# Optimization experiments

Hardware: AMD Instinct MI355X
Metric: run time of the kernel (lower is better)

## Reference

```python
import math
import jax, jax.numpy as jnp
import numpy as np

N_MARKS = 64
D_TYPE = 256      # d_type_emb (= d_k since each head module has n_head=1)
D_TIME = 256      # must be even
N_HEAD = 4
N_LAYERS = 3
D_IN = D_TYPE + D_TIME  # input dim to per-layer QKV projections
NEG = -1000000000.0
LN_EPS = 1e-5


def temporal_embedding(time):
    # time: [B,T] -> [B,T,D_TIME]; pe[...,0::2]=sin(t*div), pe[...,1::2]=cos(t*div)
    div_term = jnp.exp(jnp.arange(0, D_TIME, 2, dtype=time.dtype) * (-(math.log(10000.0) / D_TIME)))
    ang = time[..., None] * div_term  # [B,T,D_TIME//2]
    pe = jnp.stack([jnp.sin(ang), jnp.cos(ang)], axis=-1)  # interleave sin/cos
    return pe.reshape(time.shape[0], time.shape[1], D_TIME)


def layer_norm(x, w, b):
    mu = jnp.mean(x, axis=-1, keepdims=True)
    var = jnp.mean(jnp.square(x - mu), axis=-1, keepdims=True)
    return (x - mu) * jax.lax.rsqrt(var + LN_EPS) * w + b


def setup_inputs() -> dict:
    key = jax.random.key(0)
    ks = jax.random.split(key, 12)
    B, T = 4, 1024
    event_seqs = jax.random.uniform(ks[0], (B, T, N_MARKS), dtype=jnp.float32)
    time_seqs = jax.random.uniform(ks[1], (B, T), dtype=jnp.float32)
    non_pad_mask = jnp.ones((B, T, T), dtype=bool)
    s_in = 1.0 / math.sqrt(D_IN)
    s_mk = 1.0 / math.sqrt(N_MARKS)
    Wtype = jax.random.uniform(ks[2], (N_MARKS, D_TYPE), minval=-s_mk, maxval=s_mk)
    btype = jax.random.uniform(ks[3], (D_TYPE,), minval=-s_mk, maxval=s_mk)
    Wq = jax.random.uniform(ks[4], (N_HEAD, N_LAYERS, D_IN, D_TYPE), minval=-s_in, maxval=s_in)
    bq = jax.random.uniform(ks[5], (N_HEAD, N_LAYERS, D_TYPE), minval=-s_in, maxval=s_in)
    Wk = jax.random.uniform(ks[6], (N_HEAD, N_LAYERS, D_IN, D_TYPE), minval=-s_in, maxval=s_in)
    bk = jax.random.uniform(ks[7], (N_HEAD, N_LAYERS, D_TYPE), minval=-s_in, maxval=s_in)
    Wv = jax.random.uniform(ks[8], (N_HEAD, N_LAYERS, D_IN, D_TYPE), minval=-s_in, maxval=s_in)
    bv = jax.random.uniform(ks[9], (N_HEAD, N_LAYERS, D_TYPE), minval=-s_in, maxval=s_in)
    norm_w = jnp.ones((D_TYPE,), dtype=jnp.float32)
    norm_b = jnp.zeros((D_TYPE,), dtype=jnp.float32)
    return {"event_seqs": event_seqs, "time_seqs": time_seqs, "non_pad_mask": non_pad_mask,
            "Wtype": Wtype, "btype": btype, "Wq": Wq, "bq": bq, "Wk": Wk, "bk": bk,
            "Wv": Wv, "bv": bv, "norm_w": norm_w, "norm_b": norm_b}


def reference(event_seqs, time_seqs, non_pad_mask, Wtype, btype, Wq, bq, Wk, bk, Wv, bv, norm_w, norm_b):
    B, T, _ = event_seqs.shape
    # attention mask: True => masked (torch masked_fill(mask > 0, -1e9)); strict+diag upper tri
    tri = jnp.triu(jnp.ones((T, T), dtype=bool))[None]           # [1,T,T]
    attention_mask = tri & non_pad_mask                          # [B,T,T]
    layer_mask = jnp.broadcast_to(~jnp.eye(T, dtype=bool)[None], (B, T, T))
    top = jnp.concatenate([attention_mask, jnp.ones((B, T, T), dtype=bool)], axis=-1)
    bot = jnp.concatenate([attention_mask, layer_mask], axis=-1)
    combined_mask = jnp.concatenate([top, bot], axis=1)          # [B,2T,2T]

    time_emb = temporal_embedding(time_seqs)                     # [B,T,D_TIME]
    type_emb = jnp.tanh(event_seqs @ Wtype + btype)              # [B,T,D_TYPE]
    event_emb = jnp.concatenate([type_emb, time_emb], axis=-1)   # [B,T,D_IN]
    sample_time_emb = time_emb                                   # sample_times=None path
    init_cur = jnp.zeros_like(type_emb)

    scale = 1.0 / math.sqrt(D_TYPE)
    cur_layers = []
    # NOTE: event_emb is sequentially updated across layers AND heads, matching the source.
    for h in range(N_HEAD):
        cur = init_cur
        for l in range(N_LAYERS):
            x = jnp.concatenate([event_emb,
                                 jnp.concatenate([cur, sample_time_emb], axis=-1)], axis=1)  # [B,2T,D_IN]
            q = x @ Wq[h, l] + bq[h, l]
            k = x @ Wk[h, l] + bk[h, l]
            v = x @ Wv[h, l] + bv[h, l]
            scores = jnp.einsum('bqd,bkd->bqk', q, k) * scale    # [B,2T,2T]
            scores = jnp.where(combined_mask, NEG, scores)
            p = jax.nn.softmax(scores, axis=-1)
            out = jnp.einsum('bqk,bkd->bqd', p, v)               # [B,2T,D_TYPE]
            cur = jnp.tanh(out[:, T:, :]) + cur
            event_emb = jnp.concatenate([out[:, :T, :], time_emb], axis=-1)
            cur = layer_norm(cur, norm_w, norm_b)                # use_norm=True
        cur_layers.append(cur)
    return jnp.concatenate(cur_layers, axis=-1)                  # [B,T,D_TYPE*N_HEAD]
```

## Files before the change

kernel.cpp:

```cpp
#include <hip/hip_runtime.h>

typedef __attribute__((ext_vector_type(8))) short short8;
typedef __attribute__((ext_vector_type(4))) float f32x4;
typedef __attribute__((ext_vector_type(4))) unsigned short us4v;
typedef unsigned short ushort_t;
typedef unsigned int uint_t;

#define BB 4
#define T_ 1024
#define T2 2048
#define DD 256
#define DIN 512
#define NMARK 64
#define LNEPS 1e-5f
#define KDIV (-0.035977892078032f)
#define SEGL 8

__device__ __forceinline__ ushort_t f2bf(float f) {
  unsigned int u = __float_as_uint(f);
  unsigned int r = (u + 0x7fffu + ((u >> 16) & 1u)) >> 16;
  return (ushort_t)r;
}
__device__ __forceinline__ uint_t pack2(float a, float b) {
  return (uint_t)f2bf(a) | ((uint_t)f2bf(b) << 16);
}
__device__ __forceinline__ uint_t cvtpk(float lo, float hi) {
  uint_t r;
  asm("v_cvt_pk_bf16_f32 %0, %1, %2" : "=v"(r) : "v"(lo), "v"(hi));
  return r;
}

typedef const __attribute__((address_space(1))) unsigned int* as1cu32;
typedef __attribute__((address_space(3))) unsigned int* as3u32;
__device__ __forceinline__ void async_copy16(const void* g, void* l) {
  __builtin_amdgcn_global_load_lds((as1cu32)g, (as3u32)l, 16, 0, 0);
}

__global__ __launch_bounds__(256) void k_init(const float* __restrict__ ev,
                                              const float* __restrict__ tm,
                                              const float* __restrict__ Wt,
                                              const float* __restrict__ bt,
                                              ushort_t* __restrict__ Xh,
                                              float* __restrict__ Cur) {
  const int btq = blockIdx.x;
  const int b = btq >> 10;
  const int t = btq & 1023;
  const int d = threadIdx.x;
  __shared__ float evs[NMARK];
  if (d < NMARK) evs[d] = ev[(size_t)btq * NMARK + d];
  __syncthreads();
  float s = bt[d];
#pragma unroll
  for (int m = 0; m < NMARK; ++m) s += evs[m] * Wt[m * DD + d];
  const float te_type = tanhf(s);
  const float tv = tm[btq];
  const int i = d >> 1;
  const float dv = expf((float)(2 * i) * KDIV);
  const float ang = tv * dv;
  const float te_time = (d & 1) ? cosf(ang) : sinf(ang);
  ushort_t* Xb = Xh + (size_t)b * T2 * DIN;
  const ushort_t tt = f2bf(te_time);
  Xb[(size_t)t * DIN + d] = f2bf(te_type);
  Xb[(size_t)t * DIN + DD + d] = tt;
  Xb[(size_t)(T_ + t) * DIN + d] = 0;
  Xb[(size_t)(T_ + t) * DIN + DD + d] = tt;
  Cur[((size_t)b * T_ + t) * DD + d] = 0.0f;
}

__global__ __launch_bounds__(256) void k_transW(const float* __restrict__ Wq,
                                                const float* __restrict__ Wk,
                                                const float* __restrict__ Wv,
                                                ushort_t* __restrict__ WT) {
  const int mi = blockIdx.x;
  const int wsel = mi / 12, hl = mi % 12;
  const float* W = ((wsel == 0) ? Wq : (wsel == 1) ? Wk : Wv) + (size_t)hl * DIN * DD;
  const int t = blockIdx.y;
  const int k0 = (t >> 2) * 64, n0 = (t & 3) * 64;
  __shared__ float Ts[64][65];
  const int tid = threadIdx.x;
#pragma unroll
  for (int i = 0; i < 16; ++i) {
    const int idx = tid + i * 256;
    const int r = idx >> 6, c = idx & 63;
    Ts[r][c] = W[(size_t)(k0 + r) * DD + n0 + c];
  }
  __syncthreads();
  ushort_t* D = WT + (size_t)mi * DD * DIN;
#pragma unroll
  for (int i = 0; i < 16; ++i) {
    const int idx = tid + i * 256;
    const int rn = idx >> 6, ck = idx & 63;
    D[(size_t)(n0 + rn) * DIN + k0 + ck] = f2bf(Ts[ck][rn]);
  }
}

__global__ __launch_bounds__(256) void k_qkv(const ushort_t* __restrict__ Xh,
                                             const ushort_t* __restrict__ WT,
                                             const float* __restrict__ bq,
                                             const float* __restrict__ bk,
                                             const float* __restrict__ bv,
                                             ushort_t* __restrict__ Qh,
                                             ushort_t* __restrict__ Kh,
                                             ushort_t* __restrict__ VTt,
                                             int hl) {
  const int m0 = blockIdx.x * 128;
  const int n0 = blockIdx.y * 128;
  const int wsel = blockIdx.z;
  const ushort_t* Bt = WT + ((size_t)(wsel * 12 + hl)) * DD * DIN + (size_t)n0 * DIN;
  const float* bias = (wsel == 0) ? bq : (wsel == 1) ? bk : bv;

  __shared__ ushort_t As[128 * 64];
  __shared__ ushort_t Bs[128 * 64];
  const int tid = threadIdx.x;
  const int w = tid >> 6, lane = tid & 63;
  const int wr = w >> 1, wc = w & 1;
  const int lr = lane & 15, kg = lane >> 4;

  f32x4 acc[4][4];
  const f32x4 z4 = {0.f, 0.f, 0.f, 0.f};
#pragma unroll
  for (int a = 0; a < 4; ++a)
#pragma unroll
    for (int c = 0; c < 4; ++c) acc[a][c] = z4;

  for (int k0 = 0; k0 < DIN; k0 += 64) {
#pragma unroll
    for (int i = 0; i < 4; ++i) {
      const int idx = tid + i * 256;
      const int row = idx >> 3, ch = idx & 7;
      const int db = row * 128 + ((ch * 16) ^ ((row & 7) << 4));
      uint4 va = *(const uint4*)&Xh[(size_t)(m0 + row) * DIN + k0 + ch * 8];
      *(uint4*)((char*)As + db) = va;
      uint4 vb = *(const uint4*)&Bt[(size_t)row * DIN + k0 + ch * 8];
      *(uint4*)((char*)Bs + db) = vb;
    }
    __syncthreads();
#pragma unroll
    for (int kk = 0; kk < 2; ++kk) {
      short8 af[4], bfr[4];
      const int cb = kk * 64 + kg * 16;
#pragma unroll
      for (int mi = 0; mi < 4; ++mi) {
        const int row = wr * 64 + mi * 16 + lr;
        af[mi] = *(const short8*)((const char*)As + row * 128 + (cb ^ ((row & 7) << 4)));
      }
#pragma unroll
      for (int ni = 0; ni < 4; ++ni) {
        const int row = wc * 64 + ni * 16 + lr;
        bfr[ni] = *(const short8*)((const char*)Bs + row * 128 + (cb ^ ((row & 7) << 4)));
      }
#pragma unroll
      for (int mi = 0; mi < 4; ++mi)
#pragma unroll
        for (int ni = 0; ni < 4; ++ni)
          acc[mi][ni] = __builtin_amdgcn_mfma_f32_16x16x32_bf16(af[mi], bfr[ni], acc[mi][ni], 0, 0, 0);
    }
    __syncthreads();
  }

  if (wsel < 2) {
    ushort_t* C = (wsel == 0) ? Qh : Kh;
#pragma unroll
    for (int mi = 0; mi < 4; ++mi)
#pragma unroll
      for (int ni = 0; ni < 4; ++ni) {
        const int col = n0 + wc * 64 + ni * 16 + lr;
        const float bcol = bias[col];
        const int rbase = m0 + wr * 64 + mi * 16 + kg * 4;
#pragma unroll
        for (int r = 0; r < 4; ++r)
          C[(size_t)(rbase + r) * DD + col] = f2bf(acc[mi][ni][r] + bcol);
      }
  } else {
    const int b2 = m0 >> 11;
    const int t0q = m0 & 2047;
#pragma unroll
    for (int mi = 0; mi < 4; ++mi)
#pragma unroll
      for (int ni = 0; ni < 4; ++ni) {
        const int col = n0 + wc * 64 + ni * 16 + lr;
        const float bcol = bias[col];
        const int t32 = (t0q >> 5) + wr * 2 + (mi >> 1);
        const int jloc = kg * 8 + (mi & 1) * 4;
        uint2 pk;
        pk.x = pack2(acc[mi][ni][0] + bcol, acc[mi][ni][1] + bcol);
        pk.y = pack2(acc[mi][ni][2] + bcol, acc[mi][ni][3] + bcol);
        *(uint2*)(VTt + ((size_t)(b2 * 64 + t32)) * (DD * 32) + col * 32 + jloc) = pk;
      }
  }
}

__global__ __launch_bounds__(256, 2) void k_fpart(const ushort_t* __restrict__ Qh,
                                                  const ushort_t* __restrict__ Kh,
                                                  const ushort_t* __restrict__ VTt,
                                                  float* __restrict__ Cur,
                                                  ushort_t* __restrict__ Xh,
                                                  float* __restrict__ out,
                                                  const float* __restrict__ nw,
                                                  const float* __restrict__ nb,
                                                  float* __restrict__ PartO,
                                                  float* __restrict__ PartML,
                                                  int lastLayer, int h) {
  __shared__ char lds[66560];
  const int tid = threadIdx.x;
  const int bx = blockIdx.x;
  const int seg = bx >> 7;
  const int rem = bx & 127;
  const int b = rem & 3;
  const int tc = 31 - (rem >> 2);
  const int nt = tc + 2;
  const int nseg = (nt + SEGL - 1) / SEGL;
  if (seg >= nseg) return;
  const int kt0 = seg * SEGL;
  const int klen = (nt - kt0 < SEGL) ? (nt - kt0) : SEGL;
  const int dt = 32 + tc;

  const int w = tid >> 6, lane = tid & 63;
  const int kg = lane >> 4, lr = lane & 15;
  const int half = w >> 1;
  const int tq = (w & 1) * 16 + lr;
  const int t = tc * 32 + tq;
  const int r0 = (half ? T_ : 0) + t;
  const size_t bT2 = (size_t)b * T2;

  short8 qf[8];
  {
    const ushort_t* qb = Qh + (bT2 + r0) * DD + kg * 8;
#pragma unroll
    for (int kk = 0; kk < 8; ++kk) qf[kk] = *(const short8*)(qb + kk * 32);
  }

  const f32x4 z4 = {0.f, 0.f, 0.f, 0.f};
  f32x4 acc_o[16];
#pragma unroll
  for (int db = 0; db < 16; ++db) acc_o[db] = z4;
  float m_run = -1e30f, l_run = 0.f;

#define STAGE(BUF, TILE)                                                                  \
  {                                                                                       \
    const int _t = (TILE);                                                                \
    const char* Vt = (const char*)VTt + ((size_t)(b * 64 + _t)) * 16384;                  \
    _Pragma("unroll") for (int s = 0; s < 4; ++s) {                                       \
      const int c = w * 4 + s;                                                            \
      const int row2 = (c << 1) | (lane >> 5);                                            \
      const int cc2 = lane & 31;                                                          \
      async_copy16((const char*)Kh + ((bT2 + _t * 32 + row2) * DD) * 2 +                  \
                       ((cc2 * 16) ^ ((row2 & 7) << 4)),                                  \
                   lds + (BUF) * 16384 + c * 1024);                                       \
      async_copy16(Vt + c * 1024 + lane * 16,                                             \
                   lds + 32768 + (BUF) * 16384 + c * 1024);                               \
    }                                                                                     \
  }
#define TILEOF(KT) (((KT) <= tc) ? (KT) : dt)

  STAGE(0, TILEOF(kt0));

  union U8 { uint4 u; short8 s; };

  for (int ktl = 0; ktl < klen; ++ktl) {
    const int kt = kt0 + ktl;
    const int tile = TILEOF(kt);
    const bool isDiag = (kt > tc);

    if (ktl + 1 < klen) {
      STAGE((ktl + 1) & 1, TILEOF(kt + 1));
      asm volatile("s_waitcnt vmcnt(8)" ::: "memory");
    } else {
      asm volatile("s_waitcnt vmcnt(0)" ::: "memory");
    }
    __builtin_amdgcn_s_barrier();
    asm volatile("" ::: "memory");

    if (!(isDiag && half == 0)) {
      const char* KsC = lds + (ktl & 1) * 16384;
      const char* VsC = lds + 32768 + (ktl & 1) * 16384;

      f32x4 sa[2];
#pragma unroll
      for (int jb = 0; jb < 2; ++jb) {
        sa[jb] = z4;
        const int rowj = jb * 16 + lr;
        const int base = rowj * 512;
        const int swj = (rowj & 7) << 4;
#pragma unroll
        for (int kk = 0; kk < 8; ++kk) {
          short8 kf = *(const short8*)(KsC + base + ((kk * 64 + kg * 16) ^ swj));
          sa[jb] = __builtin_amdgcn_mfma_f32_16x16x32_bf16(kf, qf[kk], sa[jb], 0, 0, 0);
        }
      }

      float sv[8];
      float tmax = -1e30f;
#pragma unroll
      for (int jb = 0; jb < 2; ++jb)
#pragma unroll
        for (int rr = 0; rr < 4; ++rr) {
          const int jl = jb * 16 + kg * 4 + rr;
          const bool valid = isDiag ? (jl == tq) : ((tile * 32 + jl) < t);
          const float x = valid ? sa[jb][rr] * 0.0625f : -1e30f;
          sv[jb * 4 + rr] = x;
          tmax = fmaxf(tmax, x);
        }
      tmax = fmaxf(tmax, __shfl_xor(tmax, 16, 64));
      tmax = fmaxf(tmax, __shfl_xor(tmax, 32, 64));
      if (tmax > m_run + 8.0f) {
        const float fac = __expf(m_run - tmax);
        m_run = tmax;
        l_run *= fac;
#pragma unroll
        for (int db = 0; db < 16; ++db) acc_o[db] *= fac;
      }
      float p[8];
      float psum = 0.f;
#pragma unroll
      for (int e = 0; e < 8; ++e) {
        const float pe = (sv[e] > -1e29f) ? __expf(sv[e] - m_run) : 0.0f;
        p[e] = pe;
        psum += pe;
      }
      psum += __shfl_xor(psum, 16, 64);
      psum += __shfl_xor(psum, 32, 64);
      l_run += psum;

      U8 pf;
      pf.u.x = cvtpk(p[0], p[1]);
      pf.u.y = cvtpk(p[2], p[3]);
      pf.u.z = cvtpk(p[4], p[5]);
      pf.u.w = cvtpk(p[6], p[7]);

#pragma unroll
      for (int db = 0; db < 16; ++db) {
        U8 vf;
        vf.u = *(const uint4*)(VsC + (db * 16 + lr) * 64 + kg * 16);
        acc_o[db] = __builtin_amdgcn_mfma_f32_16x16x32_bf16(vf.s, pf.s, acc_o[db], 0, 0, 0);
      }
    }

    __builtin_amdgcn_s_barrier();
    asm volatile("" ::: "memory");
  }
#undef STAGE
#undef TILEOF

  if (nseg > 1) {
    const int slot = (b * 32 + tc) * 5 + seg;
    const int row = half * 32 + tq;
    float* pml = PartML + slot * 128;
    if (kg == 0) { pml[row] = m_run; pml[64 + row] = l_run; }
    float* po = PartO + ((size_t)slot) * (64 * 256) + row * 256 + kg * 4;
#pragma unroll
    for (int db = 0; db < 16; ++db) *(f32x4*)(po + db * 16) = acc_o[db];
    return;
  }

  const float oinv = 1.0f / l_run;

  if (!half) {
    if (t != 0) {
      ushort_t* xp = Xh + (bT2 + t) * DIN + kg * 4;
#pragma unroll
      for (int db = 0; db < 16; ++db) {
        us4v o;
#pragma unroll
        for (int rr = 0; rr < 4; ++rr) o[rr] = f2bf(acc_o[db][rr] * oinv);
        *(us4v*)(xp + db * 16) = o;
      }
    }
  } else {
    float* cp = Cur + ((size_t)b * T_ + t) * DD + kg * 4;
    float s1 = 0.f, s2 = 0.f;
#pragma unroll
    for (int db = 0; db < 16; ++db) {
      f32x4 c4 = *(const f32x4*)(cp + db * 16);
#pragma unroll
      for (int rr = 0; rr < 4; ++rr) {
        const float x = tanhf(acc_o[db][rr] * oinv) + c4[rr];
        acc_o[db][rr] = x;
        s1 += x;
        s2 += x * x;
      }
    }
    s1 += __shfl_xor(s1, 16, 64); s1 += __shfl_xor(s1, 32, 64);
    s2 += __shfl_xor(s2, 16, 64); s2 += __shfl_xor(s2, 32, 64);
    const float mean = s1 * (1.0f / 256.0f);
    const float var = s2 * (1.0f / 256.0f) - mean * mean;
    const float rinv = rsqrtf(var + LNEPS);
    ushort_t* xp = Xh + (bT2 + T_ + t) * DIN + kg * 4;
    if (lastLayer) {
      float* op = out + ((size_t)b * T_ + t) * (DD * 4) + h * DD + kg * 4;
      const us4v zz = {0, 0, 0, 0};
      const f32x4 zf = {0.f, 0.f, 0.f, 0.f};
#pragma unroll
      for (int db = 0; db < 16; ++db) {
        f32x4 w4 = *(const f32x4*)&nw[db * 16 + kg * 4];
        f32x4 b4 = *(const f32x4*)&nb[db * 16 + kg * 4];
        f32x4 y;
#pragma unroll
        for (int rr = 0; rr < 4; ++rr) y[rr] = (acc_o[db][rr] - mean) * rinv * w4[rr] + b4[rr];
        *(f32x4*)(op + db * 16) = y;
        *(f32x4*)(cp + db * 16) = zf;
        *(us4v*)(xp + db * 16) = zz;
      }
    } else {
#pragma unroll
      for (int db = 0; db < 16; ++db) {
        f32x4 w4 = *(const f32x4*)&nw[db * 16 + kg * 4];
        f32x4 b4 = *(const f32x4*)&nb[db * 16 + kg * 4];
        f32x4 y;
        us4v yh;
#pragma unroll
        for (int rr = 0; rr < 4; ++rr) {
          y[rr] = (acc_o[db][rr] - mean) * rinv * w4[rr] + b4[rr];
          yh[rr] = f2bf(y[rr]);
        }
        *(f32x4*)(cp + db * 16) = y;
        *(us4v*)(xp + db * 16) = yh;
      }
    }
  }

  if (tc < 4) {
    __syncthreads();
    float* red = (float*)(lds + 65536);
    const int col = tc * 64 + (tid & 63);
    const int q4 = tid >> 6;
    float s = 0.f;
    for (int tl = q4 * 16; tl < q4 * 16 + 16; ++tl) {
      const ushort_t* vp = VTt + ((size_t)(b * 64 + tl)) * 8192 + col * 32;
#pragma unroll
      for (int j = 0; j < 32; j += 8) {
        uint4 v = *(const uint4*)(vp + j);
        const uint_t vs[4] = {v.x, v.y, v.z, v.w};
#pragma unroll
        for (int q = 0; q < 4; ++q) {
          s += __uint_as_float(vs[q] << 16);
          s += __uint_as_float(vs[q] & 0xffff0000u);
        }
      }
    }
    red[q4 * 64 + (tid & 63)] = s;
    __syncthreads();
    if (tid < 64)
      Xh[bT2 * DIN + tc * 64 + tid] =
          f2bf((red[tid] + red[64 + tid] + red[128 + tid] + red[192 + tid]) * (1.0f / 2048.0f));
  }
}

__global__ __launch_bounds__(256) void k_merge(float* __restrict__ Cur,
                                               ushort_t* __restrict__ Xh,
                                               float* __restrict__ out,
                                               const float* __restrict__ nw,
                                               const float* __restrict__ nb,
                                               const float* __restrict__ PartO,
                                               const float* __restrict__ PartML,
                                               int lastLayer, int h) {
  const int tid = threadIdx.x;
  const int bx = blockIdx.x;
  const int b = bx & 3;
  const int tc = 7 + (bx >> 2);
  const int nt = tc + 2;
  const int nseg = (nt + SEGL - 1) / SEGL;
  const int slot0 = (b * 32 + tc) * 5;

  const int w = tid >> 6, lane = tid & 63;
  const int kg = lane >> 4, lr = lane & 15;
  const int half = w >> 1;
  const int tq = (w & 1) * 16 + lr;
  const int t = tc * 32 + tq;
  const int row = half * 32 + tq;
  const size_t bT2 = (size_t)b * T2;
  const f32x4 z4 = {0.f, 0.f, 0.f, 0.f};

  float mstar = -1e30f;
  for (int s = 0; s < nseg; ++s)
    mstar = fmaxf(mstar, PartML[(slot0 + s) * 128 + row]);
  float l_run = 0.f;
  f32x4 acc_o[16];
#pragma unroll
  for (int db = 0; db < 16; ++db) acc_o[db] = z4;
  for (int s = 0; s < nseg; ++s) {
    const float* pml = PartML + (slot0 + s) * 128;
    const float f = __expf(pml[row] - mstar);
    l_run += f * pml[64 + row];
    const float* po = PartO + ((size_t)(slot0 + s)) * (64 * 256) + row * 256 + kg * 4;
#pragma unroll
    for (int db = 0; db < 16; ++db) {
      f32x4 v = *(const f32x4*)(po + db * 16);
#pragma unroll
      for (int q = 0; q < 4; ++q) acc_o[db][q] += f * v[q];
    }
  }

  const float oinv = 1.0f / l_run;

  if (!half) {
    ushort_t* xp = Xh + (bT2 + t) * DIN + kg * 4;
#pragma unroll
    for (int db = 0; db < 16; ++db) {
      us4v o;
#pragma unroll
      for (int rr = 0; rr < 4; ++rr) o[rr] = f2bf(acc_o[db][rr] * oinv);
      *(us4v*)(xp + db * 16) = o;
    }
  } else {
    float* cp = Cur + ((size_t)b * T_ + t) * DD + kg * 4;
    float s1 = 0.f, s2 = 0.f;
#pragma unroll
    for (int db = 0; db < 16; ++db) {
      f32x4 c4 = *(const f32x4*)(cp + db * 16);
#pragma unroll
      for (int rr = 0; rr < 4; ++rr) {
        const float x = tanhf(acc_o[db][rr] * oinv) + c4[rr];
        acc_o[db][rr] = x;
        s1 += x;
        s2 += x * x;
      }
    }
    s1 += __shfl_xor(s1, 16, 64); s1 += __shfl_xor(s1, 32, 64);
    s2 += __shfl_xor(s2, 16, 64); s2 += __shfl_xor(s2, 32, 64);
    const float mean = s1 * (1.0f / 256.0f);
    const float var = s2 * (1.0f / 256.0f) - mean * mean;
    const float rinv = rsqrtf(var + LNEPS);
    ushort_t* xp = Xh + (bT2 + T_ + t) * DIN + kg * 4;
    if (lastLayer) {
      float* op = out + ((size_t)b * T_ + t) * (DD * 4) + h * DD + kg * 4;
      const us4v zz = {0, 0, 0, 0};
      const f32x4 zf = {0.f, 0.f, 0.f, 0.f};
#pragma unroll
      for (int db = 0; db < 16; ++db) {
        f32x4 w4 = *(const f32x4*)&nw[db * 16 + kg * 4];
        f32x4 b4 = *(const f32x4*)&nb[db * 16 + kg * 4];
        f32x4 y;
#pragma unroll
        for (int rr = 0; rr < 4; ++rr) y[rr] = (acc_o[db][rr] - mean) * rinv * w4[rr] + b4[rr];
        *(f32x4*)(op + db * 16) = y;
        *(f32x4*)(cp + db * 16) = zf;
        *(us4v*)(xp + db * 16) = zz;
      }
    } else {
#pragma unroll
      for (int db = 0; db < 16; ++db) {
        f32x4 w4 = *(const f32x4*)&nw[db * 16 + kg * 4];
        f32x4 b4 = *(const f32x4*)&nb[db * 16 + kg * 4];
        f32x4 y;
        us4v yh;
#pragma unroll
        for (int rr = 0; rr < 4; ++rr) {
          y[rr] = (acc_o[db][rr] - mean) * rinv * w4[rr] + b4[rr];
          yh[rr] = f2bf(y[rr]);
        }
        *(f32x4*)(cp + db * 16) = y;
        *(us4v*)(xp + db * 16) = yh;
      }
    }
  }
}

extern "C" void kernel_launch(void* const* d_in, const int* in_sizes, int n_in,
                              void* d_out, int out_size, void* d_ws, size_t ws_size,
                              hipStream_t stream) {
  const float* ev = (const float*)d_in[0];
  const float* tm = (const float*)d_in[1];
  const float* Wt = (const float*)d_in[3];
  const float* bt = (const float*)d_in[4];
  const float* Wq = (const float*)d_in[5];
  const float* bq = (const float*)d_in[6];
  const float* Wk = (const float*)d_in[7];
  const float* bk = (const float*)d_in[8];
  const float* Wv = (const float*)d_in[9];
  const float* bv = (const float*)d_in[10];
  const float* nw = (const float*)d_in[11];
  const float* nb = (const float*)d_in[12];
  float* out = (float*)d_out;

  char* p = (char*)d_ws;
  ushort_t* Xh  = (ushort_t*)p; p += (size_t)BB * T2 * DIN * 2;
  ushort_t* Qh  = (ushort_t*)p; p += (size_t)BB * T2 * DD * 2;
  ushort_t* Kh  = (ushort_t*)p; p += (size_t)BB * T2 * DD * 2;
  ushort_t* VTt = (ushort_t*)p; p += (size_t)BB * T2 * DD * 2;
  float* Cur    = (float*)p;    p += (size_t)BB * T_ * DD * 4;
  ushort_t* WT  = (ushort_t*)p; p += (size_t)36 * DD * DIN * 2;
  float* PartO  = (float*)p;    p += (size_t)640 * 64 * 256 * 4;
  float* PartML = (float*)p;

  k_init<<<BB * T_, 256, 0, stream>>>(ev, tm, Wt, bt, Xh, Cur);
  k_transW<<<dim3(36, 32), 256, 0, stream>>>(Wq, Wk, Wv, WT);

  for (int h = 0; h < 4; ++h) {
    for (int l = 0; l < 3; ++l) {
      const int hl = h * 3 + l;
      const size_t boff = (size_t)hl * DD;
      k_qkv<<<dim3(64, 2, 3), 256, 0, stream>>>(Xh, WT, bq + boff, bk + boff, bv + boff,
                                                Qh, Kh, VTt, hl);
      k_fpart<<<640, 256, 0, stream>>>(Qh, Kh, VTt, Cur, Xh, out, nw, nb,
                                       PartO, PartML, (l == 2) ? 1 : 0, h);
      k_merge<<<100, 256, 0, stream>>>(Cur, Xh, out, nw, nb,
                                       PartO, PartML, (l == 2) ? 1 : 0, h);
    }
  }
}
```

Before: 755.7 us.

## Precompute time-embedding projections once and halve QKV GEMM depth; store partials in bf16

```diff
diff --git a/kernel.cpp b/kernel.cpp
--- a/kernel.cpp
+++ b/kernel.cpp
@@ -20,6 +20,9 @@
   unsigned int u = __float_as_uint(f);
   unsigned int r = (u + 0x7fffu + ((u >> 16) & 1u)) >> 16;
   return (ushort_t)r;
+}
+__device__ __forceinline__ float bf2f(ushort_t v) {
+  return __uint_as_float(((uint_t)v) << 16);
 }
 __device__ __forceinline__ uint_t pack2(float a, float b) {
   return (uint_t)f2bf(a) | ((uint_t)f2bf(b) << 16);
@@ -94,20 +97,18 @@
   }
 }
 
-__global__ __launch_bounds__(256) void k_qkv(const ushort_t* __restrict__ Xh,
-                                             const ushort_t* __restrict__ WT,
-                                             const float* __restrict__ bq,
-                                             const float* __restrict__ bk,
-                                             const float* __restrict__ bv,
-                                             ushort_t* __restrict__ Qh,
-                                             ushort_t* __restrict__ Kh,
-                                             ushort_t* __restrict__ VTt,
-                                             int hl) {
+__global__ __launch_bounds__(256) void k_te(const ushort_t* __restrict__ Xh,
+                                            const ushort_t* __restrict__ WT,
+                                            const float* __restrict__ bq,
+                                            const float* __restrict__ bk,
+                                            const float* __restrict__ bv,
+                                            ushort_t* __restrict__ TE) {
   const int m0 = blockIdx.x * 128;
   const int n0 = blockIdx.y * 128;
-  const int wsel = blockIdx.z;
-  const ushort_t* Bt = WT + ((size_t)(wsel * 12 + hl)) * DD * DIN + (size_t)n0 * DIN;
-  const float* bias = (wsel == 0) ? bq : (wsel == 1) ? bk : bv;
+  const int mat = blockIdx.z;
+  const int wsel = mat / 12, hl = mat % 12;
+  const ushort_t* Bt = WT + (size_t)mat * DD * DIN + (size_t)n0 * DIN;
+  const float* bias = ((wsel == 0) ? bq : (wsel == 1) ? bk : bv) + hl * DD;
 
   __shared__ ushort_t As[128 * 64];
   __shared__ ushort_t Bs[128 * 64];
@@ -123,15 +124,17 @@
 #pragma unroll
     for (int c = 0; c < 4; ++c) acc[a][c] = z4;
 
-  for (int k0 = 0; k0 < DIN; k0 += 64) {
+  for (int k0 = 0; k0 < 256; k0 += 64) {
 #pragma unroll
     for (int i = 0; i < 4; ++i) {
       const int idx = tid + i * 256;
       const int row = idx >> 3, ch = idx & 7;
       const int db = row * 128 + ((ch * 16) ^ ((row & 7) << 4));
-      uint4 va = *(const uint4*)&Xh[(size_t)(m0 + row) * DIN + k0 + ch * 8];
+      const int m = m0 + row;
+      const size_t xrow = (size_t)(m >> 10) * T2 + (m & 1023);
+      uint4 va = *(const uint4*)&Xh[xrow * DIN + DD + k0 + ch * 8];
       *(uint4*)((char*)As + db) = va;
-      uint4 vb = *(const uint4*)&Bt[(size_t)row * DIN + k0 + ch * 8];
+      uint4 vb = *(const uint4*)&Bt[(size_t)row * DIN + DD + k0 + ch * 8];
       *(uint4*)((char*)Bs + db) = vb;
     }
     __syncthreads();
@@ -157,37 +160,113 @@
     }
     __syncthreads();
   }
-
-  if (wsel < 2) {
-    ushort_t* C = (wsel == 0) ? Qh : Kh;
-#pragma unroll
-    for (int mi = 0; mi < 4; ++mi)
-#pragma unroll
-      for (int ni = 0; ni < 4; ++ni) {
-        const int col = n0 + wc * 64 + ni * 16 + lr;
-        const float bcol = bias[col];
-        const int rbase = m0 + wr * 64 + mi * 16 + kg * 4;
+#pragma unroll
+  for (int mi = 0; mi < 4; ++mi)
+#pragma unroll
+    for (int ni = 0; ni < 4; ++ni) {
+      const int col = n0 + wc * 64 + ni * 16 + lr;
+      const float bcol = bias[col];
+      const int rbase = m0 + wr * 64 + mi * 16 + kg * 4;
+      us4v pk;
+#pragma unroll
+      for (int r = 0; r < 4; ++r) pk[r] = f2bf(acc[mi][ni][r] + bcol);
+      *(us4v*)&TE[((size_t)mat * DD + col) * 4096 + rbase] = pk;
+    }
+}
+
+__global__ __launch_bounds__(256) void k_qkv(const ushort_t* __restrict__ Xh,
+                                             const ushort_t* __restrict__ WT,
+                                             const ushort_t* __restrict__ TE,
+                                             ushort_t* __restrict__ Qh,
+                                             ushort_t* __restrict__ Kh,
+                                             ushort_t* __restrict__ VTt,
+                                             int hl, int curZero) {
+  const int m0 = blockIdx.x * 128;
+  const int n0 = blockIdx.y * 128;
+  const int wsel = blockIdx.z;
+  const int mat = wsel * 12 + hl;
+  const ushort_t* Bt = WT + (size_t)mat * DD * DIN + (size_t)n0 * DIN;
+  const int b2 = m0 >> 11;
+  const int mloc = m0 & 2047;
+  const bool isBottom = mloc >= 1024;
+  const int teBase = b2 * 1024 + (m0 & 1023);
+
+  __shared__ ushort_t As[128 * 64];
+  __shared__ ushort_t Bs[128 * 64];
+  const int tid = threadIdx.x;
+  const int w = tid >> 6, lane = tid & 63;
+  const int wr = w >> 1, wc = w & 1;
+  const int lr = lane & 15, kg = lane >> 4;
+
+  f32x4 acc[4][4];
+  const f32x4 z4 = {0.f, 0.f, 0.f, 0.f};
+#pragma unroll
+  for (int a = 0; a < 4; ++a)
+#pragma unroll
+    for (int c = 0; c < 4; ++c) acc[a][c] = z4;
+
+  if (!(curZero && isBottom)) {
+    for (int k0 = 0; k0 < 256; k0 += 64) {
+#pragma unroll
+      for (int i = 0; i < 4; ++i) {
+        const int idx = tid + i * 256;
+        const int row = idx >> 3, ch = idx & 7;
+        const int db = row * 128 + ((ch * 16) ^ ((row & 7) << 4));
+        uint4 va = *(const uint4*)&Xh[(size_t)(m0 + row) * DIN + k0 + ch * 8];
+        *(uint4*)((char*)As + db) = va;
+        uint4 vb = *(const uint4*)&Bt[(size_t)row * DIN + k0 + ch * 8];
+        *(uint4*)((char*)Bs + db) = vb;
+      }
+      __syncthreads();
+#pragma unroll
+      for (int kk = 0; kk < 2; ++kk) {
+        short8 af[4], bfr[4];
+        const int cb = kk * 64 + kg * 16;
+#pragma unroll
+        for (int mi = 0; mi < 4; ++mi) {
+          const int row = wr * 64 + mi * 16 + lr;
+          af[mi] = *(const short8*)((const char*)As + row * 128 + (cb ^ ((row & 7) << 4)));
+        }
+#pragma unroll
+        for (int ni = 0; ni < 4; ++ni) {
+          const int row = wc * 64 + ni * 16 + lr;
+          bfr[ni] = *(const short8*)((const char*)Bs + row * 128 + (cb ^ ((row & 7) << 4)));
+        }
+#pragma unroll
+        for (int mi = 0; mi < 4; ++mi)
+#pragma unroll
+          for (int ni = 0; ni < 4; ++ni)
+            acc[mi][ni] = __builtin_amdgcn_mfma_f32_16x16x32_bf16(af[mi], bfr[ni], acc[mi][ni], 0, 0, 0);
+      }
+      __syncthreads();
+    }
+  }
+
+#pragma unroll
+  for (int mi = 0; mi < 4; ++mi)
+#pragma unroll
+    for (int ni = 0; ni < 4; ++ni) {
+      const int col = n0 + wc * 64 + ni * 16 + lr;
+      const int rloc = wr * 64 + mi * 16 + kg * 4;
+      us4v te4 = *(const us4v*)&TE[((size_t)mat * DD + col) * 4096 + teBase + rloc];
+      float v[4];
+#pragma unroll
+      for (int r = 0; r < 4; ++r) v[r] = acc[mi][ni][r] + bf2f(te4[r]);
+      if (wsel < 2) {
+        ushort_t* C = (wsel == 0) ? Qh : Kh;
+        const int rbase = m0 + rloc;
 #pragma unroll
         for (int r = 0; r < 4; ++r)
-          C[(size_t)(rbase + r) * DD + col] = f2bf(acc[mi][ni][r] + bcol);
-      }
-  } else {
-    const int b2 = m0 >> 11;
-    const int t0q = m0 & 2047;
-#pragma unroll
-    for (int mi = 0; mi < 4; ++mi)
-#pragma unroll
-      for (int ni = 0; ni < 4; ++ni) {
-        const int col = n0 + wc * 64 + ni * 16 + lr;
-        const float bcol = bias[col];
-        const int t32 = (t0q >> 5) + wr * 2 + (mi >> 1);
+          C[(size_t)(rbase + r) * DD + col] = f2bf(v[r]);
+      } else {
+        const int t32 = (mloc >> 5) + wr * 2 + (mi >> 1);
         const int jloc = kg * 8 + (mi & 1) * 4;
         uint2 pk;
-        pk.x = pack2(acc[mi][ni][0] + bcol, acc[mi][ni][1] + bcol);
-        pk.y = pack2(acc[mi][ni][2] + bcol, acc[mi][ni][3] + bcol);
+        pk.x = pack2(v[0], v[1]);
+        pk.y = pack2(v[2], v[3]);
         *(uint2*)(VTt + ((size_t)(b2 * 64 + t32)) * (DD * 32) + col * 32 + jloc) = pk;
       }
-  }
+    }
 }
 
 __global__ __launch_bounds__(256, 2) void k_fpart(const ushort_t* __restrict__ Qh,
@@ -198,7 +277,7 @@
                                                   float* __restrict__ out,
                                                   const float* __restrict__ nw,
                                                   const float* __restrict__ nb,
-                                                  float* __restrict__ PartO,
+                                                  ushort_t* __restrict__ PartO,
                                                   float* __restrict__ PartML,
                                                   int lastLayer, int h) {
   __shared__ char lds[66560];
@@ -347,9 +426,14 @@
     const int row = half * 32 + tq;
     float* pml = PartML + slot * 128;
     if (kg == 0) { pml[row] = m_run; pml[64 + row] = l_run; }
-    float* po = PartO + ((size_t)slot) * (64 * 256) + row * 256 + kg * 4;
-#pragma unroll
-    for (int db = 0; db < 16; ++db) *(f32x4*)(po + db * 16) = acc_o[db];
+    ushort_t* po = PartO + ((size_t)slot) * (64 * 256) + row * 256 + kg * 4;
+#pragma unroll
+    for (int db = 0; db < 16; ++db) {
+      us4v o;
+#pragma unroll
+      for (int rr = 0; rr < 4; ++rr) o[rr] = f2bf(acc_o[db][rr]);
+      *(us4v*)(po + db * 16) = o;
+    }
     return;
   }
 
@@ -451,7 +535,7 @@
                                                float* __restrict__ out,
                                                const float* __restrict__ nw,
                                                const float* __restrict__ nb,
-                                               const float* __restrict__ PartO,
+                                               const ushort_t* __restrict__ PartO,
                                                const float* __restrict__ PartML,
                                                int lastLayer, int h) {
   const int tid = threadIdx.x;
@@ -482,12 +566,12 @@
     const float* pml = PartML + (slot0 + s) * 128;
     const float f = __expf(pml[row] - mstar);
     l_run += f * pml[64 + row];
-    const float* po = PartO + ((size_t)(slot0 + s)) * (64 * 256) + row * 256 + kg * 4;
+    const ushort_t* po = PartO + ((size_t)(slot0 + s)) * (64 * 256) + row * 256 + kg * 4;
 #pragma unroll
     for (int db = 0; db < 16; ++db) {
-      f32x4 v = *(const f32x4*)(po + db * 16);
-#pragma unroll
-      for (int q = 0; q < 4; ++q) acc_o[db][q] += f * v[q];
+      us4v v4 = *(const us4v*)(po + db * 16);
+#pragma unroll
+      for (int q = 0; q < 4; ++q) acc_o[db][q] += f * bf2f(v4[q]);
     }
   }
 
@@ -580,18 +664,19 @@
   ushort_t* VTt = (ushort_t*)p; p += (size_t)BB * T2 * DD * 2;
   float* Cur    = (float*)p;    p += (size_t)BB * T_ * DD * 4;
   ushort_t* WT  = (ushort_t*)p; p += (size_t)36 * DD * DIN * 2;
-  float* PartO  = (float*)p;    p += (size_t)640 * 64 * 256 * 4;
+  ushort_t* TE  = (ushort_t*)p; p += (size_t)36 * DD * 4096 * 2;
+  ushort_t* PartO = (ushort_t*)p; p += (size_t)640 * 64 * 256 * 2;
   float* PartML = (float*)p;
 
   k_init<<<BB * T_, 256, 0, stream>>>(ev, tm, Wt, bt, Xh, Cur);
   k_transW<<<dim3(36, 32), 256, 0, stream>>>(Wq, Wk, Wv, WT);
+  k_te<<<dim3(32, 2, 36), 256, 0, stream>>>(Xh, WT, bq, bk, bv, TE);
 
   for (int h = 0; h < 4; ++h) {
     for (int l = 0; l < 3; ++l) {
       const int hl = h * 3 + l;
-      const size_t boff = (size_t)hl * DD;
-      k_qkv<<<dim3(64, 2, 3), 256, 0, stream>>>(Xh, WT, bq + boff, bk + boff, bv + boff,
-                                                Qh, Kh, VTt, hl);
+      k_qkv<<<dim3(64, 2, 3), 256, 0, stream>>>(Xh, WT, TE, Qh, Kh, VTt, hl,
+                                                (l == 0) ? 1 : 0);
       k_fpart<<<640, 256, 0, stream>>>(Qh, Kh, VTt, Cur, Xh, out, nw, nb,
                                        PartO, PartML, (l == 2) ? 1 : 0, h);
       k_merge<<<100, 256, 0, stream>>>(Cur, Xh, out, nw, nb,
```

Measured after the change: 773.6 us. 1.02x slower.

## Halve QKV tile rows, skip zero cur half at layer 0, store partials as bf16

Applied to the files above, without the earlier changes.

```diff
diff --git a/kernel.cpp b/kernel.cpp
--- a/kernel.cpp
+++ b/kernel.cpp
@@ -20,6 +20,9 @@
   unsigned int u = __float_as_uint(f);
   unsigned int r = (u + 0x7fffu + ((u >> 16) & 1u)) >> 16;
   return (ushort_t)r;
+}
+__device__ __forceinline__ float bf2f(ushort_t v) {
+  return __uint_as_float(((uint_t)v) << 16);
 }
 __device__ __forceinline__ uint_t pack2(float a, float b) {
   return (uint_t)f2bf(a) | ((uint_t)f2bf(b) << 16);
@@ -102,57 +105,65 @@
                                              ushort_t* __restrict__ Qh,
                                              ushort_t* __restrict__ Kh,
                                              ushort_t* __restrict__ VTt,
-                                             int hl) {
-  const int m0 = blockIdx.x * 128;
+                                             int hl, int curZero) {
+  const int m0 = blockIdx.x * 64;
   const int n0 = blockIdx.y * 128;
   const int wsel = blockIdx.z;
   const ushort_t* Bt = WT + ((size_t)(wsel * 12 + hl)) * DD * DIN + (size_t)n0 * DIN;
-  const float* bias = (wsel == 0) ? bq : (wsel == 1) ? bk : bv;
-
-  __shared__ ushort_t As[128 * 64];
+  const float* bias = ((wsel == 0) ? bq : (wsel == 1) ? bk : bv) + hl * DD;
+  const int b2 = m0 >> 11;
+  const int mloc = m0 & 2047;
+  const bool skipHalf = curZero && (mloc >= 1024);
+
+  __shared__ ushort_t As[64 * 64];
   __shared__ ushort_t Bs[128 * 64];
   const int tid = threadIdx.x;
   const int w = tid >> 6, lane = tid & 63;
-  const int wr = w >> 1, wc = w & 1;
   const int lr = lane & 15, kg = lane >> 4;
 
-  f32x4 acc[4][4];
+  f32x4 acc[4][2];
   const f32x4 z4 = {0.f, 0.f, 0.f, 0.f};
 #pragma unroll
   for (int a = 0; a < 4; ++a)
 #pragma unroll
-    for (int c = 0; c < 4; ++c) acc[a][c] = z4;
-
-  for (int k0 = 0; k0 < DIN; k0 += 64) {
-#pragma unroll
-    for (int i = 0; i < 4; ++i) {
+    for (int c = 0; c < 2; ++c) acc[a][c] = z4;
+
+  for (int k0 = skipHalf ? 256 : 0; k0 < DIN; k0 += 64) {
+#pragma unroll
+    for (int i = 0; i < 2; ++i) {
       const int idx = tid + i * 256;
       const int row = idx >> 3, ch = idx & 7;
       const int db = row * 128 + ((ch * 16) ^ ((row & 7) << 4));
       uint4 va = *(const uint4*)&Xh[(size_t)(m0 + row) * DIN + k0 + ch * 8];
       *(uint4*)((char*)As + db) = va;
+    }
+#pragma unroll
+    for (int i = 0; i < 4; ++i) {
+      const int idx = tid + i * 256;
+      const int row = idx >> 3, ch = idx & 7;
+      const int db = row * 128 + ((ch * 16) ^ ((row & 7) << 4));
       uint4 vb = *(const uint4*)&Bt[(size_t)row * DIN + k0 + ch * 8];
       *(uint4*)((char*)Bs + db) = vb;
     }
     __syncthreads();
 #pragma unroll
     for (int kk = 0; kk < 2; ++kk) {
-      short8 af[4], bfr[4];
+      short8 af[4], bfr[2];
       const int cb = kk * 64 + kg * 16;
 #pragma unroll
       for (int mi = 0; mi < 4; ++mi) {
-        const int row = wr * 64 + mi * 16 + lr;
+        const int row = mi * 16 + lr;
         af[mi] = *(const short8*)((const char*)As + row * 128 + (cb ^ ((row & 7) << 4)));
       }
 #pragma unroll
-      for (int ni = 0; ni < 4; ++ni) {
-        const int row = wc * 64 + ni * 16 + lr;
+      for (int ni = 0; ni < 2; ++ni) {
+        const int row = w * 32 + ni * 16 + lr;
         bfr[ni] = *(const short8*)((const char*)Bs + row * 128 + (cb ^ ((row & 7) << 4)));
       }
 #pragma unroll
       for (int mi = 0; mi < 4; ++mi)
 #pragma unroll
-        for (int ni = 0; ni < 4; ++ni)
+        for (int ni = 0; ni < 2; ++ni)
           acc[mi][ni] = __builtin_amdgcn_mfma_f32_16x16x32_bf16(af[mi], bfr[ni], acc[mi][ni], 0, 0, 0);
     }
     __syncthreads();
@@ -163,24 +174,22 @@
 #pragma unroll
     for (int mi = 0; mi < 4; ++mi)
 #pragma unroll
-      for (int ni = 0; ni < 4; ++ni) {
-        const int col = n0 + wc * 64 + ni * 16 + lr;
+      for (int ni = 0; ni < 2; ++ni) {
+        const int col = n0 + w * 32 + ni * 16 + lr;
         const float bcol = bias[col];
-        const int rbase = m0 + wr * 64 + mi * 16 + kg * 4;
+        const int rbase = m0 + mi * 16 + kg * 4;
 #pragma unroll
         for (int r = 0; r < 4; ++r)
           C[(size_t)(rbase + r) * DD + col] = f2bf(acc[mi][ni][r] + bcol);
       }
   } else {
-    const int b2 = m0 >> 11;
-    const int t0q = m0 & 2047;
 #pragma unroll
     for (int mi = 0; mi < 4; ++mi)
 #pragma unroll
-      for (int ni = 0; ni < 4; ++ni) {
-        const int col = n0 + wc * 64 + ni * 16 + lr;
+      for (int ni = 0; ni < 2; ++ni) {
+        const int col = n0 + w * 32 + ni * 16 + lr;
         const float bcol = bias[col];
-        const int t32 = (t0q >> 5) + wr * 2 + (mi >> 1);
+        const int t32 = (mloc >> 5) + (mi >> 1);
         const int jloc = kg * 8 + (mi & 1) * 4;
         uint2 pk;
         pk.x = pack2(acc[mi][ni][0] + bcol, acc[mi][ni][1] + bcol);
@@ -198,7 +207,7 @@
                                                   float* __restrict__ out,
                                                   const float* __restrict__ nw,
                                                   const float* __restrict__ nb,
-                                                  float* __restrict__ PartO,
+                                                  ushort_t* __restrict__ PartO,
                                                   float* __restrict__ PartML,
                                                   int lastLayer, int h) {
   __shared__ char lds[66560];
@@ -347,9 +356,14 @@
     const int row = half * 32 + tq;
     float* pml = PartML + slot * 128;
     if (kg == 0) { pml[row] = m_run; pml[64 + row] = l_run; }
-    float* po = PartO + ((size_t)slot) * (64 * 256) + row * 256 + kg * 4;
-#pragma unroll
-    for (int db = 0; db < 16; ++db) *(f32x4*)(po + db * 16) = acc_o[db];
+    ushort_t* po = PartO + ((size_t)slot) * (64 * 256) + row * 256 + kg * 4;
+#pragma unroll
+    for (int db = 0; db < 16; ++db) {
+      us4v o;
+#pragma unroll
+      for (int rr = 0; rr < 4; ++rr) o[rr] = f2bf(acc_o[db][rr]);
+      *(us4v*)(po + db * 16) = o;
+    }
     return;
   }
 
@@ -451,7 +465,7 @@
                                                float* __restrict__ out,
                                                const float* __restrict__ nw,
                                                const float* __restrict__ nb,
-                                               const float* __restrict__ PartO,
+                                               const ushort_t* __restrict__ PartO,
                                                const float* __restrict__ PartML,
                                                int lastLayer, int h) {
   const int tid = threadIdx.x;
@@ -482,12 +496,12 @@
     const float* pml = PartML + (slot0 + s) * 128;
     const float f = __expf(pml[row] - mstar);
     l_run += f * pml[64 + row];
-    const float* po = PartO + ((size_t)(slot0 + s)) * (64 * 256) + row * 256 + kg * 4;
+    const ushort_t* po = PartO + ((size_t)(slot0 + s)) * (64 * 256) + row * 256 + kg * 4;
 #pragma unroll
     for (int db = 0; db < 16; ++db) {
-      f32x4 v = *(const f32x4*)(po + db * 16);
-#pragma unroll
-      for (int q = 0; q < 4; ++q) acc_o[db][q] += f * v[q];
+      us4v v4 = *(const us4v*)(po + db * 16);
+#pragma unroll
+      for (int q = 0; q < 4; ++q) acc_o[db][q] += f * bf2f(v4[q]);
     }
   }
 
@@ -580,7 +594,7 @@
   ushort_t* VTt = (ushort_t*)p; p += (size_t)BB * T2 * DD * 2;
   float* Cur    = (float*)p;    p += (size_t)BB * T_ * DD * 4;
   ushort_t* WT  = (ushort_t*)p; p += (size_t)36 * DD * DIN * 2;
-  float* PartO  = (float*)p;    p += (size_t)640 * 64 * 256 * 4;
+  ushort_t* PartO = (ushort_t*)p; p += (size_t)640 * 64 * 256 * 2;
   float* PartML = (float*)p;
 
   k_init<<<BB * T_, 256, 0, stream>>>(ev, tm, Wt, bt, Xh, Cur);
@@ -589,9 +603,8 @@
   for (int h = 0; h < 4; ++h) {
     for (int l = 0; l < 3; ++l) {
       const int hl = h * 3 + l;
-      const size_t boff = (size_t)hl * DD;
-      k_qkv<<<dim3(64, 2, 3), 256, 0, stream>>>(Xh, WT, bq + boff, bk + boff, bv + boff,
-                                                Qh, Kh, VTt, hl);
+      k_qkv<<<dim3(128, 2, 3), 256, 0, stream>>>(Xh, WT, bq, bk, bv, Qh, Kh, VTt, hl,
+                                                 (l == 0) ? 1 : 0);
       k_fpart<<<640, 256, 0, stream>>>(Qh, Kh, VTt, Cur, Xh, out, nw, nb,
                                        PartO, PartML, (l == 2) ? 1 : 0, h);
       k_merge<<<100, 256, 0, stream>>>(Cur, Xh, out, nw, nb,
```

Result: faster. 702.8 us (-7.0%).
